# Kernel tuning notes

Measured on AMD Instinct MI355X. Metric: run time of the kernel, lower is better.

The kernel has to match this reference:

```python
import jax, jax.numpy as jnp
import numpy as np

B, L, H = 64, 512, 512  # batch_size, input_size (src len), hidden_size


def setup_inputs() -> dict:
    key = jax.random.key(0)
    ks = jax.random.split(key, 12)
    return {
        "encoder_outputs": jax.random.normal(ks[0], (B, L, H), dtype=jnp.float32),
        "attn_mask": jax.random.randint(ks[1], (B, L), 0, 2, dtype=jnp.int64),
        "hidden": jax.random.normal(ks[2], (B, H), dtype=jnp.float32),
        "coverage": jax.random.uniform(ks[3], (B, L), dtype=jnp.float32),
        # attnLin: Linear(H, H)
        "attn_w": jax.random.normal(ks[4], (H, H), dtype=jnp.float32) * 0.02,
        "attn_b": jax.random.normal(ks[5], (H,), dtype=jnp.float32) * 0.02,
        # decoderAttnLinear: Linear(H, H)
        "dec_w": jax.random.normal(ks[6], (H, H), dtype=jnp.float32) * 0.02,
        "dec_b": jax.random.normal(ks[7], (H,), dtype=jnp.float32) * 0.02,
        # cvgConv: Conv2d(L, L, kernel=(1, H), padding='same') -> weight [L, L, 1, H]
        "cvg_w": jax.random.normal(ks[8], (L, L, 1, H), dtype=jnp.float32) * 0.02,
        "cvg_b": jax.random.normal(ks[9], (L,), dtype=jnp.float32) * 0.02,
        # v parameter (trunc_normal in torch; plain normal is fine as a baseline)
        "v": jax.random.normal(ks[10], (B, H), dtype=jnp.float32),
    }


def reference(encoder_outputs, attn_mask, hidden, coverage,
              attn_w, attn_b, dec_w, dec_b, cvg_w, cvg_b, v):
    # Per-position linear loop in torch == one batched linear over [B, L, H].
    enc_feat = jnp.einsum('blh,oh->blo', encoder_outputs, attn_w) + attn_b  # [B,L,H]
    dec_feat = (hidden @ dec_w.T + dec_b)[:, None, :]                        # [B,1,H]
    # Coverage conv: input is [B, L(channels), 1, 1]; kernel (1, H) with 'same'
    # padding means only kernel column kw = (H-1)//2 ever overlaps the single
    # real (non-zero-padded) pixel, so the conv reduces exactly to a matmul
    # with that weight column plus bias. Same math, no wasted zero-multiplies.
    center = (H - 1) // 2
    w_eff = cvg_w[:, :, 0, center]                                           # [L_out, L_in]
    cov_feat = (coverage @ w_eff.T + cvg_b)[:, :, None]                      # [B,L,1]
    feats = jnp.tanh(enc_feat + dec_feat + cov_feat)                         # [B,L,H]
    scores = jnp.einsum('blh,bh->bl', feats, v)                              # [B,L]
    scores = jnp.where(attn_mask == 1, scores, -jnp.inf)
    attn_weights = jax.nn.softmax(scores, axis=1)                            # [B,L]
    new_coverage = coverage + attn_weights                                   # coverage += aw
    context_vector = jnp.einsum('bl,blh->bh', attn_weights, encoder_outputs) # [B,H]
    return context_vector, attn_weights, new_coverage
```

## Files before the change

kernel.cpp:

```cpp
#include <hip/hip_runtime.h>

#define B_ 64
#define L_ 512
#define H_ 512
#define CENTER 255

typedef float  f32x4  __attribute__((ext_vector_type(4)));
typedef _Float16 f16x8 __attribute__((ext_vector_type(8)));
typedef unsigned short u16x4 __attribute__((ext_vector_type(4)));
typedef unsigned short u16x8 __attribute__((ext_vector_type(8)));
typedef unsigned short USH;


__device__ __forceinline__ float fast_tanh(float x) {
    float e = __expf(2.0f * x);
    return 1.0f - 2.0f * __builtin_amdgcn_rcpf(e + 1.0f);
}

__launch_bounds__(512)
__global__ void pre_kernel(const float* __restrict__ cvg_w, const float* __restrict__ cvg_b,
                           const float* __restrict__ coverage,
                           const float* __restrict__ aw, USH* __restrict__ bh16,
                           const float* __restrict__ hidden, const float* __restrict__ dec_w,
                           const float* __restrict__ dec_b,
                           float* __restrict__ dec_feat, float* __restrict__ cov_feat) {
    __shared__ float wl2[1024];
    __shared__ float cs[512 * 65];
    __shared__ float sbuf[512];
    __shared__ float pr[512];
    const int bid = blockIdx.x, t = threadIdx.x;
    const int i0 = bid, i1 = bid + 256;

    wl2[t]       = cvg_w[((size_t)(i0 * L_ + t)) * H_ + CENTER];
    wl2[512 + t] = cvg_w[((size_t)(i1 * L_ + t)) * H_ + CENTER];

    if (t < 256) {
        int i = bid * 256 + t;
        float4 x = *(const float4*)&aw[(size_t)i * 4];
        float xs[4] = {x.x, x.y, x.z, x.w};
        u16x4 h;
        #pragma unroll
        for (int j = 0; j < 4; ++j)
            h[j] = __builtin_bit_cast(USH, (_Float16)xs[j]);
        *(u16x4*)&bh16[(size_t)i * 4] = h;
    }

    const int b = bid >> 2, qq = bid & 3;
    const int ol = t & 127, part = t >> 7;
    sbuf[t] = hidden[b * H_ + t];
    __syncthreads();

    {
        const float* row  = dec_w + (size_t)(qq * 128 + ol) * H_ + part * 128;
        const float* hseg = sbuf + part * 128;
        float d0 = 0.f, d1 = 0.f, d2 = 0.f, d3 = 0.f;
        #pragma unroll
        for (int k = 0; k < 128; k += 16) {
            float4 w0 = *(const float4*)&row[k];
            float4 w1 = *(const float4*)&row[k + 4];
            float4 w2 = *(const float4*)&row[k + 8];
            float4 w3 = *(const float4*)&row[k + 12];
            d0 += w0.x * hseg[k]      + w0.y * hseg[k + 1]  + w0.z * hseg[k + 2]  + w0.w * hseg[k + 3];
            d1 += w1.x * hseg[k + 4]  + w1.y * hseg[k + 5]  + w1.z * hseg[k + 6]  + w1.w * hseg[k + 7];
            d2 += w2.x * hseg[k + 8]  + w2.y * hseg[k + 9]  + w2.z * hseg[k + 10] + w2.w * hseg[k + 11];
            d3 += w3.x * hseg[k + 12] + w3.y * hseg[k + 13] + w3.z * hseg[k + 14] + w3.w * hseg[k + 15];
        }
        pr[t] = d0 + d1 + d2 + d3;
    }

    #pragma unroll 8
    for (int c = 0; c < 64; ++c)
        cs[t * 65 + c] = coverage[c * L_ + t];
    __syncthreads();

    if (t < 128)
        dec_feat[b * H_ + qq * 128 + t] = pr[t] + pr[t + 128] + pr[t + 256] + pr[t + 384]
                                          + dec_b[qq * 128 + t];

    {
        const int bb = t >> 3, jg = t & 7;
        float s0 = 0.f, s1 = 0.f;
        #pragma unroll 8
        for (int jj = 0; jj < 64; ++jj) {
            int j = jg * 64 + ((jj + jg * 8) & 63);
            float c = cs[j * 65 + bb];
            s0 += c * wl2[j];
            s1 += c * wl2[512 + j];
        }
        s0 += __shfl_xor(s0, 1, 64);
        s0 += __shfl_xor(s0, 2, 64);
        s0 += __shfl_xor(s0, 4, 64);
        s1 += __shfl_xor(s1, 1, 64);
        s1 += __shfl_xor(s1, 2, 64);
        s1 += __shfl_xor(s1, 4, 64);
        if (jg == 0) {
            cov_feat[bb * L_ + i0] = s0 + cvg_b[i0];
            cov_feat[bb * L_ + i1] = s1 + cvg_b[i1];
        }
    }
}

#define BM 128

#define STAGE_B(BUF, KS1)                                                                  \
    {                                                                                      \
        _Pragma("unroll")                                                                  \
        for (int it = 0; it < 2; ++it)                                                     \
            __builtin_amdgcn_global_load_lds(                                              \
                (const __attribute__((address_space(1))) void*)(bh16 + goffB[it] + (KS1) * 32), \
                (__attribute__((address_space(3))) void*)&Bsh[BUF][(wv * 2 + it) * 512],   \
                16, 0, 0);                                                                 \
    }

#define CVTWRITEA2(BUF, A4a, A4b)                                                          \
    {                                                                                      \
        float axs[8] = {A4a.x, A4a.y, A4a.z, A4a.w, A4b.x, A4b.y, A4b.z, A4b.w};           \
        u16x8 hh;                                                                          \
        _Pragma("unroll")                                                                  \
        for (int j = 0; j < 8; ++j)                                                        \
            hh[j] = __builtin_bit_cast(USH, (_Float16)axs[j]);                             \
        *(u16x8*)&Ash[BUF][awoff] = hh;                                                    \
    }

__launch_bounds__(512, 4)
__global__ void fused_score_mfma(const float* __restrict__ enc,
                                 const USH* __restrict__ bh16,
                                 const float* __restrict__ attn_b,
                                 const float* __restrict__ dec_feat,
                                 const float* __restrict__ cov_feat,
                                 const float* __restrict__ v,
                                 float* __restrict__ spart) {
    __shared__ USH Bsh[3][8192];
    __shared__ USH Ash[2][4096];

    const int t  = threadIdx.x;
    const int wv = t >> 6, ln = t & 63;
    const int wr = wv >> 2, wc = wv & 3;
    const int q  = ln >> 4, cl = ln & 15;
    const int mt = blockIdx.x, half = blockIdx.y;
    const int m0 = mt * BM;
    const int b  = mt >> 2;
    const int n0 = half * 256;

    int goffB[2];
    #pragma unroll
    for (int it = 0; it < 2; ++it) {
        int c   = wv * 2 + it;
        int srl = ln >> 3;
        int u   = (ln & 7) ^ (srl & 7);
        int n   = n0 + c * 16 + srl * 2 + (u >> 2);
        goffB[it] = n * 512 + (u & 3) * 8;
    }
    const int sA   = (((cl & 1) * 4 + q) ^ ((cl >> 1) & 7)) * 8;
    const int aoff = wr * 2048 + (cl >> 1) * 64 + sA;
    const int boff = wc * 2048 + (cl >> 1) * 64 + sA;

    const int arow = t >> 2, ak4 = t & 3;
    const int asw  = ((arow & 1) * 4 + ak4) ^ ((arow >> 1) & 7);
    const int awoff = (arow >> 1) * 64 + asw * 8;
    const float* agsrc = enc + (size_t)(m0 + arow) * H_ + ak4 * 8;

    f32x4 acc[4][4];
    #pragma unroll
    for (int mf = 0; mf < 4; ++mf)
        #pragma unroll
        for (int nf = 0; nf < 4; ++nf) acc[mf][nf] = (f32x4){0.f, 0.f, 0.f, 0.f};

    float4 aPa = *(const float4*)(agsrc + 32);
    float4 aPb = *(const float4*)(agsrc + 36);
    float4 c0a = *(const float4*)agsrc;
    float4 c0b = *(const float4*)(agsrc + 4);
    __builtin_amdgcn_sched_barrier(0);
    STAGE_B(0, 0);
    STAGE_B(1, 1);
    __builtin_amdgcn_sched_barrier(0);
    CVTWRITEA2(0, c0a, c0b);
    asm volatile("s_waitcnt lgkmcnt(0)" ::: "memory");
    asm volatile("s_waitcnt vmcnt(2)" ::: "memory");
    __builtin_amdgcn_sched_barrier(0);
    __builtin_amdgcn_s_barrier();

    #pragma unroll
    for (int ks = 0; ks < 16; ++ks) {
        const int curB = ks % 3;
        const int curA = ks & 1, nxtA = curA ^ 1;
        float4 aNa, aNb;
        if (ks < 14) {
            STAGE_B((ks + 2) % 3, ks + 2);
            aNa = *(const float4*)(agsrc + (ks + 2) * 32);
            aNb = *(const float4*)(agsrc + (ks + 2) * 32 + 4);
            __builtin_amdgcn_sched_barrier(0);
        }

        f16x8 ah[4];
        #pragma unroll
        for (int mf = 0; mf < 4; ++mf)
            ah[mf] = *(const f16x8*)&Ash[curA][aoff + mf * 512];
        __builtin_amdgcn_s_setprio(1);
        #pragma unroll
        for (int nf = 0; nf < 4; ++nf) {
            f16x8 bh = *(const f16x8*)&Bsh[curB][boff + nf * 512];
            #pragma unroll
            for (int mf = 0; mf < 4; ++mf)
                acc[mf][nf] = __builtin_amdgcn_mfma_f32_16x16x32_f16(ah[mf], bh, acc[mf][nf], 0, 0, 0);
        }
        __builtin_amdgcn_s_setprio(0);

        if (ks < 15) {
            CVTWRITEA2(nxtA, aPa, aPb);
            aPa = aNa; aPb = aNb;
            asm volatile("s_waitcnt lgkmcnt(0)" ::: "memory");
            if (ks < 14)
                asm volatile("s_waitcnt vmcnt(4)" ::: "memory");
            else
                asm volatile("s_waitcnt vmcnt(0)" ::: "memory");
            __builtin_amdgcn_sched_barrier(0);
            __builtin_amdgcn_s_barrier();
        }
    }
    __syncthreads();

    float (*scred)[BM] = (float (*)[BM])Ash;
    float addv[4], vvv[4];
    #pragma unroll
    for (int nf = 0; nf < 4; ++nf) {
        int n = n0 + wc * 64 + nf * 16 + cl;
        addv[nf] = attn_b[n] + dec_feat[b * H_ + n];
        vvv[nf]  = v[b * H_ + n];
    }
    #pragma unroll
    for (int mf = 0; mf < 4; ++mf) {
        #pragma unroll
        for (int reg = 0; reg < 4; ++reg) {
            int row = wr * 64 + mf * 16 + q * 4 + reg;
            float cf = cov_feat[m0 + row];
            float s = 0.f;
            #pragma unroll
            for (int nf = 0; nf < 4; ++nf)
                s += fast_tanh(acc[mf][nf][reg] + addv[nf] + cf) * vvv[nf];
            s += __shfl_xor(s, 1, 64);
            s += __shfl_xor(s, 2, 64);
            s += __shfl_xor(s, 4, 64);
            s += __shfl_xor(s, 8, 64);
            if (cl == 0) scred[wc][row] = s;
        }
    }
    __syncthreads();
    if (t < BM) {
        float s = 0.f;
        #pragma unroll
        for (int g = 0; g < 4; ++g) s += scred[g][t];
        spart[half * (B_ * L_) + m0 + t] = s;
    }
}

__launch_bounds__(1024)
__global__ void smctx_kernel(const float* __restrict__ spart, const int* __restrict__ mask,
                             const float* __restrict__ coverage, const float* __restrict__ enc,
                             float* __restrict__ out) {
    __shared__ float w[512];
    __shared__ float red[16];
    __shared__ float red2[16];
    __shared__ float4 cred4[32][32];
    __shared__ float4 cmid[4][32];
    const int bid = blockIdx.x, b = bid >> 2, hc = bid & 3, t = threadIdx.x;
    const int wv = t >> 6, ln = t & 63;

    float sv = 0.f; bool mk = false;
    if (t < 512) {
        mk = (mask[b * L_ + t] == 1);
        sv = spart[b * L_ + t] + spart[B_ * L_ + b * L_ + t];
    }
    float val = (t < 512 && mk) ? sv : -INFINITY;

    float r = val;
    #pragma unroll
    for (int d = 1; d <= 32; d <<= 1) r = fmaxf(r, __shfl_xor(r, d, 64));
    if (ln == 0) red[wv] = r;
    __syncthreads();
    float gmax = red[0];
    #pragma unroll
    for (int i = 1; i < 16; ++i) gmax = fmaxf(gmax, red[i]);

    float p = (t < 512 && mk) ? __expf(sv - gmax) : 0.f;
    float qq = p;
    #pragma unroll
    for (int d = 1; d <= 32; d <<= 1) qq += __shfl_xor(qq, d, 64);
    if (ln == 0) red2[wv] = qq;
    __syncthreads();
    float tot = 0.f;
    #pragma unroll
    for (int i = 0; i < 16; ++i) tot += red2[i];

    float wt = p / tot;
    if (t < 512) {
        w[t] = wt;
        if (hc == 0) {
            out[B_ * H_ + b * L_ + t] = wt;
            out[B_ * H_ + B_ * L_ + b * L_ + t] = coverage[b * L_ + t] + wt;
        }
    }
    __syncthreads();

    const int c4 = t & 31, rg = t >> 5;
    const float4* ebase = (const float4*)enc
                          + ((size_t)(b * L_ + rg)) * 128 + hc * 32 + c4;
    float4 a4 = {0.f, 0.f, 0.f, 0.f};
    #pragma unroll
    for (int k = 0; k < 16; ++k) {
        float wl_ = w[rg + 32 * k];
        float4 e = ebase[(size_t)(32 * k) * 128];
        a4.x += wl_ * e.x; a4.y += wl_ * e.y; a4.z += wl_ * e.z; a4.w += wl_ * e.w;
    }
    cred4[rg][c4] = a4;
    __syncthreads();
    if (t < 128) {
        const int gq = t >> 5;
        float4 s = {0.f, 0.f, 0.f, 0.f};
        #pragma unroll
        for (int g = 0; g < 8; ++g) {
            float4 c = cred4[gq * 8 + g][c4];
            s.x += c.x; s.y += c.y; s.z += c.z; s.w += c.w;
        }
        cmid[gq][c4] = s;
    }
    __syncthreads();
    if (t < 32) {
        float4 s = {0.f, 0.f, 0.f, 0.f};
        #pragma unroll
        for (int g = 0; g < 4; ++g) {
            float4 c = cmid[g][t];
            s.x += c.x; s.y += c.y; s.z += c.z; s.w += c.w;
        }
        *(float4*)&out[b * H_ + hc * 128 + t * 4] = s;
    }
}

extern "C" void kernel_launch(void* const* d_in, const int* in_sizes, int n_in,
                              void* d_out, int out_size, void* d_ws, size_t ws_size,
                              hipStream_t stream) {
    const float* enc      = (const float*)d_in[0];
    const int*   mask     = (const int*)d_in[1];
    const float* hidden   = (const float*)d_in[2];
    const float* coverage = (const float*)d_in[3];
    const float* attn_w   = (const float*)d_in[4];
    const float* attn_b   = (const float*)d_in[5];
    const float* dec_w    = (const float*)d_in[6];
    const float* dec_b    = (const float*)d_in[7];
    const float* cvg_w    = (const float*)d_in[8];
    const float* cvg_b    = (const float*)d_in[9];
    const float* v        = (const float*)d_in[10];
    float* out = (float*)d_out;
    float* ws  = (float*)d_ws;
    float* dec_feat = ws + 32768;
    float* cov_feat = ws + 65536;
    float* spart    = ws + 98304;
    USH* bpk = (USH*)(ws + 360448);

    hipLaunchKernelGGL(pre_kernel,       dim3(256),     dim3(512),  0, stream,
                       cvg_w, cvg_b, coverage, attn_w, bpk, hidden, dec_w, dec_b,
                       dec_feat, cov_feat);
    hipLaunchKernelGGL(fused_score_mfma, dim3(256, 2),  dim3(512),  0, stream,
                       enc, bpk, attn_b, dec_feat, cov_feat, v, spart);
    hipLaunchKernelGGL(smctx_kernel,     dim3(256),     dim3(1024), 0, stream,
                       spart, mask, coverage, enc, out);
}
```

Measured before the change: 64.71 us.

## Pre-convert encoder outputs to fp16 and stage A tiles via direct global-to-LDS loads

Adds an fp32-to-fp16 conversion of the full encoder_outputs tensor to the pre-kernel and writes the result to workspace. The MFMA score kernel then loads A tiles straight into LDS with global_load_lds, triple-buffered like B, instead of loading fp32 into registers and converting in-loop. This is meant to remove register traffic and conversion work from the main loop and to halve the A bytes each of the two column-half blocks reads. The cost is an extra full pass over the 64 MB encoder tensor (read fp32, write fp16) in the pre-kernel, plus more LDS per block.

New measurement: 75.91 us. 1.17x slower.

```diff
diff --git a/kernel.cpp b/kernel.cpp
--- a/kernel.cpp
+++ b/kernel.cpp
@@ -21,6 +21,7 @@
 __global__ void pre_kernel(const float* __restrict__ cvg_w, const float* __restrict__ cvg_b,
                            const float* __restrict__ coverage,
                            const float* __restrict__ aw, USH* __restrict__ bh16,
+                           const float* __restrict__ enc, USH* __restrict__ enc16,
                            const float* __restrict__ hidden, const float* __restrict__ dec_w,
                            const float* __restrict__ dec_b,
                            float* __restrict__ dec_feat, float* __restrict__ cov_feat) {
@@ -45,6 +46,22 @@
         *(u16x4*)&bh16[(size_t)i * 4] = h;
     }
 
+    {
+        const float4* e4 = (const float4*)enc;
+        u16x4* o4 = (u16x4*)enc16;
+        #pragma unroll 4
+        for (int k = 0; k < 32; ++k) {
+            int idx = bid * 16384 + k * 512 + t;
+            float4 x = e4[idx];
+            float xs[4] = {x.x, x.y, x.z, x.w};
+            u16x4 h;
+            #pragma unroll
+            for (int j = 0; j < 4; ++j)
+                h[j] = __builtin_bit_cast(USH, (_Float16)xs[j]);
+            o4[idx] = h;
+        }
+    }
+
     const int b = bid >> 2, qq = bid & 3;
     const int ol = t & 127, part = t >> 7;
     sbuf[t] = hidden[b * H_ + t];
@@ -102,7 +119,7 @@
 
 #define BM 128
 
-#define STAGE_B(BUF, KS1)                                                                  \
+#define STAGE_AB(BUF, KS1)                                                                 \
     {                                                                                      \
         _Pragma("unroll")                                                                  \
         for (int it = 0; it < 2; ++it)                                                     \
@@ -110,20 +127,14 @@
                 (const __attribute__((address_space(1))) void*)(bh16 + goffB[it] + (KS1) * 32), \
                 (__attribute__((address_space(3))) void*)&Bsh[BUF][(wv * 2 + it) * 512],   \
                 16, 0, 0);                                                                 \
-    }
-
-#define CVTWRITEA2(BUF, A4a, A4b)                                                          \
-    {                                                                                      \
-        float axs[8] = {A4a.x, A4a.y, A4a.z, A4a.w, A4b.x, A4b.y, A4b.z, A4b.w};           \
-        u16x8 hh;                                                                          \
-        _Pragma("unroll")                                                                  \
-        for (int j = 0; j < 8; ++j)                                                        \
-            hh[j] = __builtin_bit_cast(USH, (_Float16)axs[j]);                             \
-        *(u16x8*)&Ash[BUF][awoff] = hh;                                                    \
+        __builtin_amdgcn_global_load_lds(                                                  \
+            (const __attribute__((address_space(1))) void*)(enc16 + goffA + (KS1) * 32),   \
+            (__attribute__((address_space(3))) void*)&Ash[BUF][wv * 512],                  \
+            16, 0, 0);                                                                     \
     }
 
 __launch_bounds__(512, 4)
-__global__ void fused_score_mfma(const float* __restrict__ enc,
+__global__ void fused_score_mfma(const USH* __restrict__ enc16,
                                  const USH* __restrict__ bh16,
                                  const float* __restrict__ attn_b,
                                  const float* __restrict__ dec_feat,
@@ -131,7 +142,7 @@
                                  const float* __restrict__ v,
                                  float* __restrict__ spart) {
     __shared__ USH Bsh[3][8192];
-    __shared__ USH Ash[2][4096];
+    __shared__ USH Ash[3][4096];
 
     const int t  = threadIdx.x;
     const int wv = t >> 6, ln = t & 63;
@@ -151,55 +162,44 @@
         int n   = n0 + c * 16 + srl * 2 + (u >> 2);
         goffB[it] = n * 512 + (u & 3) * 8;
     }
+    int goffA;
+    {
+        int x    = (ln & 7) ^ (ln >> 3);
+        int arw  = wv * 16 + (ln >> 3) * 2 + (x >> 2);
+        goffA = (m0 + arw) * 512 + (x & 3) * 8;
+    }
     const int sA   = (((cl & 1) * 4 + q) ^ ((cl >> 1) & 7)) * 8;
     const int aoff = wr * 2048 + (cl >> 1) * 64 + sA;
     const int boff = wc * 2048 + (cl >> 1) * 64 + sA;
 
-    const int arow = t >> 2, ak4 = t & 3;
-    const int asw  = ((arow & 1) * 4 + ak4) ^ ((arow >> 1) & 7);
-    const int awoff = (arow >> 1) * 64 + asw * 8;
-    const float* agsrc = enc + (size_t)(m0 + arow) * H_ + ak4 * 8;
-
     f32x4 acc[4][4];
     #pragma unroll
     for (int mf = 0; mf < 4; ++mf)
         #pragma unroll
         for (int nf = 0; nf < 4; ++nf) acc[mf][nf] = (f32x4){0.f, 0.f, 0.f, 0.f};
 
-    float4 aPa = *(const float4*)(agsrc + 32);
-    float4 aPb = *(const float4*)(agsrc + 36);
-    float4 c0a = *(const float4*)agsrc;
-    float4 c0b = *(const float4*)(agsrc + 4);
+    STAGE_AB(0, 0);
+    STAGE_AB(1, 1);
     __builtin_amdgcn_sched_barrier(0);
-    STAGE_B(0, 0);
-    STAGE_B(1, 1);
-    __builtin_amdgcn_sched_barrier(0);
-    CVTWRITEA2(0, c0a, c0b);
-    asm volatile("s_waitcnt lgkmcnt(0)" ::: "memory");
-    asm volatile("s_waitcnt vmcnt(2)" ::: "memory");
+    asm volatile("s_waitcnt vmcnt(3)" ::: "memory");
     __builtin_amdgcn_sched_barrier(0);
     __builtin_amdgcn_s_barrier();
 
     #pragma unroll
     for (int ks = 0; ks < 16; ++ks) {
-        const int curB = ks % 3;
-        const int curA = ks & 1, nxtA = curA ^ 1;
-        float4 aNa, aNb;
-        if (ks < 14) {
-            STAGE_B((ks + 2) % 3, ks + 2);
-            aNa = *(const float4*)(agsrc + (ks + 2) * 32);
-            aNb = *(const float4*)(agsrc + (ks + 2) * 32 + 4);
-            __builtin_amdgcn_sched_barrier(0);
-        }
+        const int cur = ks % 3;
+        if (ks < 14)
+            STAGE_AB((ks + 2) % 3, ks + 2);
+        __builtin_amdgcn_sched_barrier(0);
 
         f16x8 ah[4];
         #pragma unroll
         for (int mf = 0; mf < 4; ++mf)
-            ah[mf] = *(const f16x8*)&Ash[curA][aoff + mf * 512];
+            ah[mf] = *(const f16x8*)&Ash[cur][aoff + mf * 512];
         __builtin_amdgcn_s_setprio(1);
         #pragma unroll
         for (int nf = 0; nf < 4; ++nf) {
-            f16x8 bh = *(const f16x8*)&Bsh[curB][boff + nf * 512];
+            f16x8 bh = *(const f16x8*)&Bsh[cur][boff + nf * 512];
             #pragma unroll
             for (int mf = 0; mf < 4; ++mf)
                 acc[mf][nf] = __builtin_amdgcn_mfma_f32_16x16x32_f16(ah[mf], bh, acc[mf][nf], 0, 0, 0);
@@ -207,11 +207,8 @@
         __builtin_amdgcn_s_setprio(0);
 
         if (ks < 15) {
-            CVTWRITEA2(nxtA, aPa, aPb);
-            aPa = aNa; aPb = aNb;
-            asm volatile("s_waitcnt lgkmcnt(0)" ::: "memory");
             if (ks < 14)
-                asm volatile("s_waitcnt vmcnt(4)" ::: "memory");
+                asm volatile("s_waitcnt vmcnt(3)" ::: "memory");
             else
                 asm volatile("s_waitcnt vmcnt(0)" ::: "memory");
             __builtin_amdgcn_sched_barrier(0);
@@ -355,13 +352,14 @@
     float* dec_feat = ws + 32768;
     float* cov_feat = ws + 65536;
     float* spart    = ws + 98304;
-    USH* bpk = (USH*)(ws + 360448);
+    USH* bpk   = (USH*)(ws + 360448);
+    USH* enc16 = (USH*)(ws + 1048576);
 
     hipLaunchKernelGGL(pre_kernel,       dim3(256),     dim3(512),  0, stream,
-                       cvg_w, cvg_b, coverage, attn_w, bpk, hidden, dec_w, dec_b,
-                       dec_feat, cov_feat);
+                       cvg_w, cvg_b, coverage, attn_w, bpk, enc, enc16, hidden,
+                       dec_w, dec_b, dec_feat, cov_feat);
     hipLaunchKernelGGL(fused_score_mfma, dim3(256, 2),  dim3(512),  0, stream,
-                       enc, bpk, attn_b, dec_feat, cov_feat, v, spart);
+                       enc16, bpk, attn_b, dec_feat, cov_feat, v, spart);
     hipLaunchKernelGGL(smctx_kernel,     dim3(256),     dim3(1024), 0, stream,
                        spart, mask, coverage, enc, out);
 }
```
